# Kernel tuning notes

Measured on AMD Instinct MI355X. Metric: run time of the kernel, lower is better.

The kernel has to match this reference:

```python
import jax, jax.numpy as jnp
import numpy as np

EMB_DIM = 32
N_FACET = 8
EPS = 1e-12  # torch F.normalize eps

def _l2_normalize(v, axis):
    n = jnp.linalg.norm(v, axis=axis, keepdims=True)
    return v / jnp.maximum(n, EPS)

def setup_inputs() -> dict:
    key = jax.random.key(0)
    k1, k2 = jax.random.split(key)
    features = jax.random.normal(k1, (128, 16, N_FACET * EMB_DIM), dtype=jnp.float32)
    neigh_features = jax.random.normal(k2, (128, 16, 64, N_FACET * EMB_DIM), dtype=jnp.float32)
    return {"features": features, "neigh_features": neigh_features}

def reference(features, neigh_features):
    B, N, D = features.shape
    K = neigh_features.shape[2]
    x = features.reshape(B, N, N_FACET, EMB_DIM)              # [B,N,F,E]
    z = neigh_features.reshape(B, N, K, N_FACET, EMB_DIM)     # [B,N,K,F,E]
    x = _l2_normalize(x, axis=3)
    z = _l2_normalize(z, axis=4)
    # cosine similarity scores over emb dim: [B,N,K,F]
    a = jnp.einsum('bnkfe,bnfe->bnkf', z, x)
    a = jax.nn.softmax(a, axis=2)  # softmax over neighbors
    # weighted sum over neighbors: [B,N,F,E]
    u = jnp.einsum('bnkfe,bnkf->bnfe', z, a)
    return u.reshape(B, N, N_FACET * EMB_DIM)
```

## Files before the change

### kernel.cpp

```cpp
#include <hip/hip_runtime.h>
#include <math.h>


#define EMB 32
#define NF 8
#define DD 256
#define KK 64

typedef float nfloat4 __attribute__((ext_vector_type(4)));

__global__ __launch_bounds__(256)
void homo_attn_kernel(const float* __restrict__ features,
                      const float* __restrict__ neigh,
                      float* __restrict__ out)
{
    const int bn = blockIdx.x;
    const int t  = threadIdx.x;
    const int l  = t & 63;
    const int tg = t >> 6;
    const int f  = l >> 3;
    const int sub = l & 7;

    const float* xp = features + (size_t)bn * DD;
    const float* zp = neigh    + (size_t)bn * (KK * DD);

    nfloat4 xv = ((const nfloat4*)xp)[l];
    nfloat4 zr[16];
#pragma unroll
    for (int i = 0; i < 16; ++i) {
        const int k = i * 4 + tg;
        zr[i] = __builtin_nontemporal_load(((const nfloat4*)(zp + k * DD)) + l);
    }
    __builtin_amdgcn_sched_barrier(0);

    float ss = xv.x*xv.x + xv.y*xv.y + xv.z*xv.z + xv.w*xv.w;
    ss += __shfl_xor(ss, 1);
    ss += __shfl_xor(ss, 2);
    ss += __shfl_xor(ss, 4);
    float xs = 1.0f / fmaxf(sqrtf(ss), 1e-12f);
    xv *= xs;

    __shared__ float   a_s[KK * NF];
    __shared__ nfloat4 part[4][64];

#pragma unroll
    for (int i = 0; i < 16; ++i) {
        const int k = i * 4 + tg;
        nfloat4 z = zr[i];
        float zss = z.x*z.x + z.y*z.y + z.z*z.z + z.w*z.w;
        zss += __shfl_xor(zss, 1);
        zss += __shfl_xor(zss, 2);
        zss += __shfl_xor(zss, 4);
        float zs = 1.0f / fmaxf(sqrtf(zss), 1e-12f);
        z *= zs;
        zr[i] = z;
        float d = z.x*xv.x + z.y*xv.y + z.z*xv.z + z.w*xv.w;
        d += __shfl_xor(d, 1);
        d += __shfl_xor(d, 2);
        d += __shfl_xor(d, 4);
        if (sub == 0) a_s[k * NF + f] = d;
    }
    __syncthreads();

    float m = -1e30f;
#pragma unroll 8
    for (int k = 0; k < KK; ++k) m = fmaxf(m, a_s[k * NF + f]);
    float denom = 0.0f;
#pragma unroll 8
    for (int k = 0; k < KK; ++k) denom += __expf(a_s[k * NF + f] - m);

    nfloat4 u = (nfloat4)(0.f, 0.f, 0.f, 0.f);
#pragma unroll
    for (int i = 0; i < 16; ++i) {
        const int k = i * 4 + tg;
        const float w = __expf(a_s[k * NF + f] - m);
        u += w * zr[i];
    }
    part[tg][l] = u;
    __syncthreads();

    if (tg == 0) {
        nfloat4 r = part[0][l] + part[1][l] + part[2][l] + part[3][l];
        r *= (1.0f / denom);
        __builtin_nontemporal_store(r, ((nfloat4*)(out + (size_t)bn * DD)) + l);
    }
}

extern "C" void kernel_launch(void* const* d_in, const int* in_sizes, int n_in,
                              void* d_out, int out_size, void* d_ws, size_t ws_size,
                              hipStream_t stream) {
    const float* features = (const float*)d_in[0];
    const float* neigh    = (const float*)d_in[1];
    float* out            = (float*)d_out;
    const int BN = in_sizes[0] / DD;
    homo_attn_kernel<<<BN, 256, 0, stream>>>(features, neigh, out);
}
```

Measured before the change: 195.9 us.

## Split attention into separate score and weighted-sum kernels

Replaces the single fused kernel with two kernels. The first computes cosine scores and inverse neighbor norms with one wave per neighbor row. The second applies softmax and accumulates the weighted sum by reloading the neighbor rows, folding the normalization into the per-neighbor weights. The split is meant to raise parallelism and lower register pressure from holding 16 vectors per thread. In exchange, the 128 MB neighbor tensor is read twice from memory, which likely dominates in a bandwidth-bound kernel, and the workspace offset is hardcoded to 2048 rows.

```diff
diff --git a/kernel.cpp b/kernel.cpp
--- a/kernel.cpp
+++ b/kernel.cpp
@@ -2,64 +2,64 @@
 #include <math.h>
 
 
-#define EMB 32
 #define NF 8
 #define DD 256
 #define KK 64
 
-typedef float nfloat4 __attribute__((ext_vector_type(4)));
+typedef float f4 __attribute__((ext_vector_type(4)));
 
 __global__ __launch_bounds__(256)
-void homo_attn_kernel(const float* __restrict__ features,
-                      const float* __restrict__ neigh,
-                      float* __restrict__ out)
+void scores_kernel(const float* __restrict__ features,
+                   const float* __restrict__ neigh,
+                   float* __restrict__ scores,
+                   float* __restrict__ zinv)
+{
+    const int gw  = (blockIdx.x * 256 + threadIdx.x) >> 6;
+    const int l   = threadIdx.x & 63;
+    const int f   = l >> 3;
+    const int sub = l & 7;
+    const int bn  = gw >> 6;
+
+    const f4 z = ((const f4*)(neigh    + (size_t)gw * DD))[l];
+    const f4 x = ((const f4*)(features + (size_t)bn * DD))[l];
+
+    float zss = z.x*z.x + z.y*z.y + z.z*z.z + z.w*z.w;
+    float xss = x.x*x.x + x.y*x.y + x.z*x.z + x.w*x.w;
+    float dot = z.x*x.x + z.y*x.y + z.z*x.z + z.w*x.w;
+#pragma unroll
+    for (int s = 1; s <= 4; s <<= 1) {
+        zss += __shfl_xor(zss, s);
+        xss += __shfl_xor(xss, s);
+        dot += __shfl_xor(dot, s);
+    }
+    const float zn = fmaxf(sqrtf(zss), 1e-12f);
+    const float xn = fmaxf(sqrtf(xss), 1e-12f);
+    if (sub == 0) scores[(size_t)gw * NF + f] = dot / (zn * xn);
+    if (sub == 1) zinv  [(size_t)gw * NF + f] = 1.0f / zn;
+}
+
+__global__ __launch_bounds__(256)
+void attend_kernel(const float* __restrict__ neigh,
+                   const float* __restrict__ scores,
+                   const float* __restrict__ zinv,
+                   float* __restrict__ out)
 {
     const int bn = blockIdx.x;
     const int t  = threadIdx.x;
     const int l  = t & 63;
     const int tg = t >> 6;
     const int f  = l >> 3;
-    const int sub = l & 7;
 
-    const float* xp = features + (size_t)bn * DD;
-    const float* zp = neigh    + (size_t)bn * (KK * DD);
+    __shared__ float a_s[KK * NF];
+    __shared__ float zi_s[KK * NF];
+    __shared__ f4    part[4][64];
 
-    nfloat4 xv = ((const nfloat4*)xp)[l];
-    nfloat4 zr[16];
-#pragma unroll
-    for (int i = 0; i < 16; ++i) {
-        const int k = i * 4 + tg;
-        zr[i] = __builtin_nontemporal_load(((const nfloat4*)(zp + k * DD)) + l);
-    }
-    __builtin_amdgcn_sched_barrier(0);
-
-    float ss = xv.x*xv.x + xv.y*xv.y + xv.z*xv.z + xv.w*xv.w;
-    ss += __shfl_xor(ss, 1);
-    ss += __shfl_xor(ss, 2);
-    ss += __shfl_xor(ss, 4);
-    float xs = 1.0f / fmaxf(sqrtf(ss), 1e-12f);
-    xv *= xs;
-
-    __shared__ float   a_s[KK * NF];
-    __shared__ nfloat4 part[4][64];
-
-#pragma unroll
-    for (int i = 0; i < 16; ++i) {
-        const int k = i * 4 + tg;
-        nfloat4 z = zr[i];
-        float zss = z.x*z.x + z.y*z.y + z.z*z.z + z.w*z.w;
-        zss += __shfl_xor(zss, 1);
-        zss += __shfl_xor(zss, 2);
-        zss += __shfl_xor(zss, 4);
-        float zs = 1.0f / fmaxf(sqrtf(zss), 1e-12f);
-        z *= zs;
-        zr[i] = z;
-        float d = z.x*xv.x + z.y*xv.y + z.z*xv.z + z.w*xv.w;
-        d += __shfl_xor(d, 1);
-        d += __shfl_xor(d, 2);
-        d += __shfl_xor(d, 4);
-        if (sub == 0) a_s[k * NF + f] = d;
-    }
+    const float* sp = scores + (size_t)bn * (KK * NF);
+    const float* zp = zinv   + (size_t)bn * (KK * NF);
+    a_s [t]       = sp[t];
+    a_s [t + 256] = sp[t + 256];
+    zi_s[t]       = zp[t];
+    zi_s[t + 256] = zp[t + 256];
     __syncthreads();
 
     float m = -1e30f;
@@ -68,21 +68,29 @@
     float denom = 0.0f;
 #pragma unroll 8
     for (int k = 0; k < KK; ++k) denom += __expf(a_s[k * NF + f] - m);
+    const float inv = 1.0f / denom;
 
-    nfloat4 u = (nfloat4)(0.f, 0.f, 0.f, 0.f);
+    float wk[16];
 #pragma unroll
     for (int i = 0; i < 16; ++i) {
         const int k = i * 4 + tg;
-        const float w = __expf(a_s[k * NF + f] - m);
-        u += w * zr[i];
+        wk[i] = __expf(a_s[k * NF + f] - m) * inv * zi_s[k * NF + f];
+    }
+
+    const float* zrow = neigh + (size_t)bn * (KK * DD);
+    f4 u = (f4)(0.f, 0.f, 0.f, 0.f);
+#pragma unroll
+    for (int i = 0; i < 16; ++i) {
+        const int k = i * 4 + tg;
+        const f4 zv = ((const f4*)(zrow + k * DD))[l];
+        u += wk[i] * zv;
     }
     part[tg][l] = u;
     __syncthreads();
 
     if (tg == 0) {
-        nfloat4 r = part[0][l] + part[1][l] + part[2][l] + part[3][l];
-        r *= (1.0f / denom);
-        __builtin_nontemporal_store(r, ((nfloat4*)(out + (size_t)bn * DD)) + l);
+        f4 r = part[0][l] + part[1][l] + part[2][l] + part[3][l];
+        ((f4*)(out + (size_t)bn * DD))[l] = r;
     }
 }
 
@@ -92,6 +100,12 @@
     const float* features = (const float*)d_in[0];
     const float* neigh    = (const float*)d_in[1];
     float* out            = (float*)d_out;
+
+    float* scores = (float*)d_ws;
+    float* zinvp  = scores + (size_t)2048 * KK * NF;
+
     const int BN = in_sizes[0] / DD;
-    homo_attn_kernel<<<BN, 256, 0, stream>>>(features, neigh, out);
+    const int nwavesA = BN * KK;
+    scores_kernel<<<nwavesA / 4, 256, 0, stream>>>(features, neigh, scores, zinvp);
+    attend_kernel<<<BN, 256, 0, stream>>>(neigh, scores, zinvp, out);
 }
```

Result: slower. 210.3 us (+7.3%).
